# Optimization experiments

Hardware: AMD Instinct MI355X
Metric: run time of the kernel (lower is better)

Reference implementation:

```python
import jax, jax.numpy as jnp
import numpy as np

H = 2048
N = 2_097_152
BINS = 256


def _tensor2image(x):
    # de-normalize from [-1,1]-style to [0,1] (SCGAN's tensor2image)
    return x * 0.5 + 0.5


def _cdf(vals):
    # torch.histc(vals, bins=256, min=0, max=256): unit-width bins; values here lie in [0,256)
    b = jnp.clip(jnp.floor(vals), 0, BINS - 1).astype(jnp.int32)
    hist = jnp.zeros((BINS,), jnp.float32).at[b].add(1.0)
    c = jnp.cumsum(hist)
    return c / c[BINS - 1]


def _trans_table(ref_cdf, adj_cdf):
    # table[i] = first j in 1..255 with adj[j-1] <= ref[i] <= adj[j]; else i. table[0]=0, table[255]=255.
    r = ref_cdf[:, None]                # [256,1]
    lo = adj_cdf[None, :-1]             # adj[j-1], j=1..255
    hi = adj_cdf[None, 1:]              # adj[j]
    cond = (lo <= r) & (r <= hi)        # [256,255]
    found = jnp.any(cond, axis=1)
    j_first = 1 + jnp.argmax(cond, axis=1)
    table = jnp.where(found, j_first, jnp.arange(BINS))
    table = table.at[0].set(0).at[BINS - 1].set(BINS - 1)
    return table


def _histogram_matching(dst_img, ref_img, i0, i1, i2, i3):
    dst_align = dst_img[:, i0, i1]      # [3,N]
    ref_align = ref_img[:, i2, i3]      # [3,N]
    cdf_dst = jax.vmap(_cdf)(dst_align)           # [3,256]
    cdf_ref = jax.vmap(_cdf)(ref_align)           # [3,256]
    tables = jax.vmap(_trans_table)(cdf_dst, cdf_ref)  # [3,256] int
    ix = jnp.clip(jnp.floor(dst_align), 0, BINS - 1).astype(jnp.int32)
    matched = jnp.take_along_axis(tables, ix, axis=1).astype(dst_img.dtype)  # [3,N]
    return dst_img.at[:, i0, i1].set(matched)


def setup_inputs() -> dict:
    key = jax.random.key(0)
    ks = jax.random.split(key, 9)
    return {
        "input_data": jax.random.uniform(ks[0], (1, 3, H, H), jnp.float32),
        "target_data": jax.random.uniform(ks[1], (1, 3, H, H), jnp.float32),
        "mask_src": jax.random.randint(ks[2], (1, 1, H, H), 0, 2).astype(jnp.float32),
        "mask_tar": jax.random.randint(ks[3], (1, 1, H, H), 0, 2).astype(jnp.float32),
        "idx0": jax.random.randint(ks[4], (N,), 0, H),
        "idx1": jax.random.randint(ks[5], (N,), 0, H),
        "idx2": jax.random.randint(ks[6], (N,), 0, H),
        "idx3": jax.random.randint(ks[7], (N,), 0, H),
        "ref": jax.random.uniform(ks[8], (1, 3, H, H), jnp.float32),
    }


def reference(input_data, target_data, mask_src, mask_tar, idx0, idx1, idx2, idx3, ref):
    img = _tensor2image(input_data)[0] * 255.0   # [3,H,H]
    tgt = _tensor2image(target_data)[0] * 255.0  # [3,H,H]
    rf = _tensor2image(ref)[0] * 255.0           # [3,H,H]
    m_src = jnp.broadcast_to(mask_src[0, 0], img.shape)
    m_tar = jnp.broadcast_to(mask_tar[0, 0], tgt.shape)
    input_masked = img * m_src
    target_masked = tgt * m_tar
    ref_masked = rf * m_src
    match = jax.lax.stop_gradient(
        _histogram_matching(ref_masked, target_masked, idx0, idx1, idx2, idx3)
    ) * m_src
    return jnp.mean(jnp.abs(input_masked - match))
```

## Files before the change

### kernel.cpp

```cpp
#include <hip/hip_runtime.h>

#define H 2048
#define HH (H * H)
#define NIDX 2097152
#define BINS 256
#define CH 3

#define NBUCK 64
#define NLIST 128
#define CAPG  139264
#define WS_HIST_DST 0
#define WS_HIST_REF 3072
#define WS_TABLE    6144
#define WS_ACC      9216
#define WS_CURS     9728
#define WS_CTRL_BYTES 16384
#define WS_SEL      16384
#define WS_BPS      (16384 + (size_t)HH)
#define WS_BPR      (WS_BPS + (size_t)HH * 4)
#define WS_LIST     (WS_BPR + (size_t)HH * 4)
#define WS_MAIN_BYTES (WS_LIST + (size_t)NLIST * CAPG * 2)

#define FB_CNT_DST  16384
#define FB_BINPACK  (16384 + (size_t)HH * 2)
#define FB_ZERO_BYTES (16384 + (size_t)HH * 2)

__device__ __forceinline__ int bin_of(float v) {
    int b = (int)floorf(v);
    return min(max(b, 0), BINS - 1);
}


__global__ __launch_bounds__(256) void prep_main(
    const float* __restrict__ mask_src, const float* __restrict__ mask_tar,
    const float* __restrict__ refimg, const float* __restrict__ tgtimg,
    unsigned int* __restrict__ bps, unsigned int* __restrict__ bpr,
    unsigned int* __restrict__ sel4)
{
    const int nq = HH / 4;
    const int stride = gridDim.x * 256;
    for (int q = blockIdx.x * 256 + threadIdx.x; q < nq; q += stride) {
        float4 ms4 = ((const float4*)mask_src)[q];
        float4 mt4 = ((const float4*)mask_tar)[q];
        const float ms[4] = { ms4.x, ms4.y, ms4.z, ms4.w };
        const float mt[4] = { mt4.x, mt4.y, mt4.z, mt4.w };
        unsigned int wsrc[4] = { 0u, 0u, 0u, 0u };
        unsigned int wref[4] = { 0u, 0u, 0u, 0u };
        #pragma unroll
        for (int c = 0; c < CH; ++c) {
            float4 r4 = ((const float4*)(refimg + (size_t)c * HH))[q];
            float4 t4 = ((const float4*)(tgtimg + (size_t)c * HH))[q];
            const float rr[4] = { r4.x, r4.y, r4.z, r4.w };
            const float tt[4] = { t4.x, t4.y, t4.z, t4.w };
            #pragma unroll
            for (int e = 0; e < 4; ++e) {
                float vs = (rr[e] * 0.5f + 0.5f) * 255.0f * ms[e];
                float vt = (tt[e] * 0.5f + 0.5f) * 255.0f * mt[e];
                wsrc[e] |= ((unsigned int)bin_of(vs)) << (8 * c);
                wref[e] |= ((unsigned int)bin_of(vt)) << (8 * c);
            }
        }
        uint4 o1 = { wsrc[0], wsrc[1], wsrc[2], wsrc[3] };
        uint4 o2 = { wref[0], wref[1], wref[2], wref[3] };
        ((uint4*)bps)[q] = o1;
        ((uint4*)bpr)[q] = o2;
        sel4[q] = 0u;
    }
}

#define P1_BLOCKS 512
#define P1_SPB (NIDX / P1_BLOCKS)
#define P1_CAP 128

__global__ __launch_bounds__(256) void partition_kernel(
    const int* __restrict__ idx0, const int* __restrict__ idx1,
    const int* __restrict__ idx2, const int* __restrict__ idx3,
    unsigned short* __restrict__ list_g, unsigned int* __restrict__ curs)
{
    __shared__ unsigned short stage[NLIST * P1_CAP];
    __shared__ unsigned int lcnt[NLIST];
    __shared__ unsigned int lbase[NLIST];
    for (int i = threadIdx.x; i < NLIST; i += 256) lcnt[i] = 0u;
    __syncthreads();

    const int base_k = blockIdx.x * P1_SPB;
    for (int r = 0; r < P1_SPB / 256; ++r) {
        int k = base_k + r * 256 + threadIdx.x;
        int pd = idx0[k] * H + idx1[k];
        int pr = idx2[k] * H + idx3[k];
        {
            int l = pd >> 16;
            unsigned int pos = atomicAdd(&lcnt[l], 1u);
            if (pos < P1_CAP) stage[l * P1_CAP + pos] = (unsigned short)(pd & 0xFFFF);
            else {
                unsigned int g = atomicAdd(&curs[l], 1u);
                if (g < CAPG) list_g[(size_t)l * CAPG + g] = (unsigned short)(pd & 0xFFFF);
            }
        }
        {
            int l = 64 + (pr >> 16);
            unsigned int pos = atomicAdd(&lcnt[l], 1u);
            if (pos < P1_CAP) stage[l * P1_CAP + pos] = (unsigned short)(pr & 0xFFFF);
            else {
                unsigned int g = atomicAdd(&curs[l], 1u);
                if (g < CAPG) list_g[(size_t)l * CAPG + g] = (unsigned short)(pr & 0xFFFF);
            }
        }
    }
    __syncthreads();
    if (threadIdx.x < NLIST) {
        unsigned int n = min(lcnt[threadIdx.x], (unsigned int)P1_CAP);
        lbase[threadIdx.x] = atomicAdd(&curs[threadIdx.x], n);
    }
    __syncthreads();
    for (int b = 0; b < NLIST; ++b) {
        int n = (int)min(lcnt[b], (unsigned int)P1_CAP);
        unsigned int gb = lbase[b];
        for (int e = threadIdx.x; e < n; e += 256) {
            unsigned int gi = gb + e;
            if (gi < CAPG) list_g[(size_t)b * CAPG + gi] = stage[b * P1_CAP + e];
        }
    }
}

__global__ __launch_bounds__(256) void gather_hist_kernel(
    const unsigned short* __restrict__ list_g, const unsigned int* __restrict__ curs,
    const unsigned int* __restrict__ bps, const unsigned int* __restrict__ bpr,
    unsigned char* __restrict__ selected,
    unsigned int* __restrict__ hist_dst, unsigned int* __restrict__ hist_ref)
{
    __shared__ unsigned int hh[CH * BINS];
    for (int i = threadIdx.x; i < CH * BINS; i += 256) hh[i] = 0u;
    __syncthreads();

    const int xcd  = blockIdx.x & 7;
    const int j    = blockIdx.x >> 3;
    const int bsl  = j & 15;
    const int sub  = j >> 4;
    const int side = bsl >> 3;
    const int bucket = xcd * 8 + (bsl & 7);
    const int l = side * 64 + bucket;
    const unsigned int pbase = ((unsigned int)bucket) << 16;
    const unsigned int* __restrict__ src = side ? bpr : bps;

    const unsigned int n = min(curs[l], (unsigned int)CAPG);
    const unsigned int chunk = (((n + 15u) >> 4) + 7u) & ~7u;
    const unsigned int s = (unsigned int)sub * chunk;
    const unsigned int e = min(s + chunk, n);
    const unsigned short* lbase = list_g + (size_t)l * CAPG;

    unsigned int zc = 0;
    for (unsigned int ib = s + (unsigned int)threadIdx.x * 8u; ib < e; ib += 2048u) {
        unsigned int w[8];
        unsigned int pcnt;
        if (ib + 8u <= e) {
            uint4 raw = *(const uint4*)(lbase + ib);
            const unsigned int ent[8] = {
                raw.x & 0xFFFFu, raw.x >> 16, raw.y & 0xFFFFu, raw.y >> 16,
                raw.z & 0xFFFFu, raw.z >> 16, raw.w & 0xFFFFu, raw.w >> 16 };
            #pragma unroll
            for (int k = 0; k < 8; ++k) {
                unsigned int p = pbase | ent[k];
                w[k] = src[p];
                if (side == 0) selected[p] = 1;
            }
            pcnt = 8u;
        } else {
            pcnt = e - ib;
            #pragma unroll
            for (int k = 0; k < 8; ++k) {
                if ((unsigned int)k < pcnt) {
                    unsigned int p = pbase | (unsigned int)lbase[ib + k];
                    w[k] = src[p];
                    if (side == 0) selected[p] = 1;
                } else w[k] = 0xFFFFFFFFu;
            }
        }
        #pragma unroll
        for (int k = 0; k < 8; ++k) {
            if ((unsigned int)k < pcnt) {
                unsigned int ww = w[k];
                if (ww == 0u) ++zc;
                else {
                    atomicAdd(&hh[0 * BINS + (ww & 0xFFu)], 1u);
                    atomicAdd(&hh[1 * BINS + ((ww >> 8) & 0xFFu)], 1u);
                    atomicAdd(&hh[2 * BINS + ((ww >> 16) & 0xFFu)], 1u);
                }
            }
        }
    }

    int z = (int)zc;
    #pragma unroll
    for (int off = 32; off; off >>= 1) z += __shfl_down(z, off);
    if ((threadIdx.x & 63) == 0 && z) {
        atomicAdd(&hh[0 * BINS], (unsigned int)z);
        atomicAdd(&hh[1 * BINS], (unsigned int)z);
        atomicAdd(&hh[2 * BINS], (unsigned int)z);
    }

    __syncthreads();
    unsigned int* dsthist = side ? hist_ref : hist_dst;
    for (int i = threadIdx.x; i < CH * BINS; i += 256) {
        unsigned int v = hh[i];
        if (v) atomicAdd(&dsthist[i], v);
    }
}

__global__ __launch_bounds__(256) void table_kernel(
    const unsigned int* __restrict__ hist_dst,
    const unsigned int* __restrict__ hist_ref,
    int* __restrict__ table)
{
    __shared__ float cd[CH * BINS];
    __shared__ float cr[CH * BINS];
    __shared__ float wpart[4];
    const int i = threadIdx.x;
    const int lane = i & 63;
    const int wave = i >> 6;

    for (int a = 0; a < 6; ++a) {
        const unsigned int* h = (a < 3) ? (hist_dst + a * BINS) : (hist_ref + (a - 3) * BINS);
        float* out = (a < 3) ? (cd + a * BINS) : (cr + (a - 3) * BINS);
        float x = (float)h[i];
        #pragma unroll
        for (int off = 1; off < 64; off <<= 1) {
            float y = __shfl_up(x, off);
            if (lane >= off) x += y;
        }
        if (lane == 63) wpart[wave] = x;
        __syncthreads();
        float prefix = 0.0f;
        #pragma unroll
        for (int w = 0; w < 3; ++w) if (w < wave) prefix += wpart[w];
        x += prefix;
        float tot = wpart[0] + wpart[1] + wpart[2] + wpart[3];
        out[i] = x / tot;
        __syncthreads();
    }

    #pragma unroll
    for (int c = 0; c < CH; ++c) {
        int t;
        if (i == 0) t = 0;
        else if (i == BINS - 1) t = BINS - 1;
        else {
            float r = cd[c * BINS + i];
            int lo = 1, hi = BINS - 1;
            while (lo < hi) {
                int mid = (lo + hi) >> 1;
                if (cr[c * BINS + mid] < r) lo = mid + 1; else hi = mid;
            }
            t = (cr[c * BINS + lo - 1] <= r) ? lo : i;
        }
        table[c * BINS + i] = t;
    }
}

__global__ __launch_bounds__(256) void loss_sel_kernel(
    const float* __restrict__ input, const float* __restrict__ refimg,
    const float* __restrict__ mask_src, const unsigned char* __restrict__ selected,
    const int* __restrict__ table, double* __restrict__ acc)
{
    __shared__ int tab[CH * BINS];
    for (int i = threadIdx.x; i < CH * BINS; i += 256) tab[i] = table[i];
    __syncthreads();

    float lsum = 0.0f;
    const int nq = HH / 4;
    const int stride = gridDim.x * 256;
    for (int q = blockIdx.x * 256 + threadIdx.x; q < nq; q += stride) {
        float4 m4 = ((const float4*)mask_src)[q];
        uchar4 s4 = ((const uchar4*)selected)[q];
        const unsigned char ss[4] = { s4.x, s4.y, s4.z, s4.w };
        const float mm[4] = { m4.x, m4.y, m4.z, m4.w };
        #pragma unroll
        for (int c = 0; c < CH; ++c) {
            float4 a4 = ((const float4*)(input + (size_t)c * HH))[q];
            float4 r4 = ((const float4*)(refimg + (size_t)c * HH))[q];
            const float aa[4] = { a4.x, a4.y, a4.z, a4.w };
            const float rr[4] = { r4.x, r4.y, r4.z, r4.w };
            #pragma unroll
            for (int e = 0; e < 4; ++e) {
                float m = mm[e];
                float av = (aa[e] * 0.5f + 0.5f) * 255.0f * m;
                float rv = (rr[e] * 0.5f + 0.5f) * 255.0f * m;
                float tv = (float)tab[c * BINS + bin_of(rv)];
                float mv = m * (ss[e] ? tv : rv);
                lsum += fabsf(av - mv);
            }
        }
    }

    double d = (double)lsum;
    #pragma unroll
    for (int off = 32; off; off >>= 1) d += __shfl_down(d, off);
    __shared__ double wsum[4];
    int wid = threadIdx.x >> 6;
    int lane = threadIdx.x & 63;
    if (lane == 0) wsum[wid] = d;
    __syncthreads();
    if (threadIdx.x == 0) {
        double t = wsum[0] + wsum[1] + wsum[2] + wsum[3];
        atomicAdd(acc, t);
    }
}

__global__ void finalize_kernel(const double* __restrict__ acc, float* __restrict__ out)
{
    if (threadIdx.x == 0 && blockIdx.x == 0) {
        out[0] = (float)(acc[0] / (double)(CH * (double)HH));
    }
}


__device__ __forceinline__ void cnt_inc(unsigned int* cnt, int p) {
    atomicAdd(&cnt[p >> 1], (p & 1) ? 0x10000u : 1u);
}

__global__ __launch_bounds__(256) void fb_prep_kernel(
    const float* __restrict__ mask_tar, const float* __restrict__ tgtimg,
    unsigned int* __restrict__ binpack)
{
    const int nq = HH / 4;
    const int stride = gridDim.x * 256;
    for (int q = blockIdx.x * 256 + threadIdx.x; q < nq; q += stride) {
        float4 m4 = ((const float4*)mask_tar)[q];
        const float mm[4] = { m4.x, m4.y, m4.z, m4.w };
        unsigned int w[4] = { 0u, 0u, 0u, 0u };
        #pragma unroll
        for (int c = 0; c < CH; ++c) {
            float4 t4 = ((const float4*)(tgtimg + (size_t)c * HH))[q];
            const float tt[4] = { t4.x, t4.y, t4.z, t4.w };
            #pragma unroll
            for (int e = 0; e < 4; ++e) {
                float v = (tt[e] * 0.5f + 0.5f) * 255.0f * mm[e];
                w[e] |= ((unsigned int)bin_of(v)) << (8 * c);
            }
        }
        uint4 out = { w[0], w[1], w[2], w[3] };
        ((uint4*)binpack)[q] = out;
    }
}

__global__ __launch_bounds__(256) void fb_scatter_kernel(
    const int4* __restrict__ idx0, const int4* __restrict__ idx1,
    const int4* __restrict__ idx2, const int4* __restrict__ idx3,
    const unsigned int* __restrict__ binpack,
    unsigned int* __restrict__ cnt_dst, unsigned int* __restrict__ hist_ref)
{
    __shared__ unsigned int hr[CH * BINS];
    for (int i = threadIdx.x; i < CH * BINS; i += 256) hr[i] = 0u;
    __syncthreads();

    unsigned int zc = 0;
    const int n4 = NIDX / 4;
    const int stride = gridDim.x * 256;
    for (int k = blockIdx.x * 256 + threadIdx.x; k < n4; k += stride) {
        int4 a = idx0[k], b = idx1[k], c = idx2[k], d = idx3[k];
        int p0 = c.x * H + d.x, p1 = c.y * H + d.y;
        int p2 = c.z * H + d.z, p3 = c.w * H + d.w;
        unsigned int w0 = binpack[p0], w1 = binpack[p1];
        unsigned int w2 = binpack[p2], w3 = binpack[p3];

        cnt_inc(cnt_dst, a.x * H + b.x);
        cnt_inc(cnt_dst, a.y * H + b.y);
        cnt_inc(cnt_dst, a.z * H + b.z);
        cnt_inc(cnt_dst, a.w * H + b.w);

        const unsigned int ws2[4] = { w0, w1, w2, w3 };
        #pragma unroll
        for (int e = 0; e < 4; ++e) {
            unsigned int w = ws2[e];
            if (w == 0u) ++zc;
            else {
                atomicAdd(&hr[0 * BINS + (w & 0xFFu)], 1u);
                atomicAdd(&hr[1 * BINS + ((w >> 8) & 0xFFu)], 1u);
                atomicAdd(&hr[2 * BINS + ((w >> 16) & 0xFFu)], 1u);
            }
        }
    }

    int z = (int)zc;
    #pragma unroll
    for (int off = 32; off; off >>= 1) z += __shfl_down(z, off);
    if ((threadIdx.x & 63) == 0 && z) {
        atomicAdd(&hr[0 * BINS], (unsigned int)z);
        atomicAdd(&hr[1 * BINS], (unsigned int)z);
        atomicAdd(&hr[2 * BINS], (unsigned int)z);
    }

    __syncthreads();
    for (int i = threadIdx.x; i < CH * BINS; i += 256) {
        unsigned int v = hr[i];
        if (v) atomicAdd(&hist_ref[i], v);
    }
}

__global__ __launch_bounds__(256) void fb_sweep_kernel(
    const float* __restrict__ mask_src, const float* __restrict__ refimg,
    const unsigned int* __restrict__ cnt_dst,
    unsigned int* __restrict__ hist_dst)
{
    __shared__ unsigned int hd[CH * BINS];
    for (int i = threadIdx.x; i < CH * BINS; i += 256) hd[i] = 0u;
    __syncthreads();

    unsigned int zc = 0;
    const int nq = HH / 4;
    const int stride = gridDim.x * 256;
    for (int q = blockIdx.x * 256 + threadIdx.x; q < nq; q += stride) {
        uint2 wd = ((const uint2*)cnt_dst)[q];
        unsigned int cdc[4] = { wd.x & 0xFFFFu, wd.x >> 16, wd.y & 0xFFFFu, wd.y >> 16 };
        float4 ms4 = ((const float4*)mask_src)[q];
        const float ms[4] = { ms4.x, ms4.y, ms4.z, ms4.w };

        float rv[CH][4];
        #pragma unroll
        for (int c = 0; c < CH; ++c) {
            float4 r4 = ((const float4*)(refimg + (size_t)c * HH))[q];
            rv[c][0] = r4.x; rv[c][1] = r4.y; rv[c][2] = r4.z; rv[c][3] = r4.w;
        }
        #pragma unroll
        for (int e = 0; e < 4; ++e) {
            if (cdc[e]) {
                if (ms[e] == 0.0f) zc += cdc[e];
                else {
                    #pragma unroll
                    for (int c = 0; c < CH; ++c) {
                        float v = (rv[c][e] * 0.5f + 0.5f) * 255.0f;
                        atomicAdd(&hd[c * BINS + bin_of(v)], cdc[e]);
                    }
                }
            }
        }
    }

    int z = (int)zc;
    #pragma unroll
    for (int off = 32; off; off >>= 1) z += __shfl_down(z, off);
    if ((threadIdx.x & 63) == 0 && z) {
        atomicAdd(&hd[0 * BINS], (unsigned int)z);
        atomicAdd(&hd[1 * BINS], (unsigned int)z);
        atomicAdd(&hd[2 * BINS], (unsigned int)z);
    }

    __syncthreads();
    for (int i = threadIdx.x; i < CH * BINS; i += 256) {
        unsigned int v = hd[i];
        if (v) atomicAdd(&hist_dst[i], v);
    }
}

__global__ __launch_bounds__(256) void fb_loss_kernel(
    const float* __restrict__ input, const float* __restrict__ refimg,
    const float* __restrict__ mask_src, const unsigned int* __restrict__ cnt_dst,
    const int* __restrict__ table, double* __restrict__ acc)
{
    __shared__ int tab[CH * BINS];
    for (int i = threadIdx.x; i < CH * BINS; i += 256) tab[i] = table[i];
    __syncthreads();

    float lsum = 0.0f;
    const int nq = HH / 4;
    const int stride = gridDim.x * 256;
    for (int q = blockIdx.x * 256 + threadIdx.x; q < nq; q += stride) {
        float4 m4 = ((const float4*)mask_src)[q];
        uint2 w = ((const uint2*)cnt_dst)[q];
        const unsigned int sel[4] = { w.x & 0xFFFFu, w.x >> 16, w.y & 0xFFFFu, w.y >> 16 };
        const float mm[4] = { m4.x, m4.y, m4.z, m4.w };
        #pragma unroll
        for (int c = 0; c < CH; ++c) {
            float4 a4 = ((const float4*)(input + (size_t)c * HH))[q];
            float4 r4 = ((const float4*)(refimg + (size_t)c * HH))[q];
            const float aa[4] = { a4.x, a4.y, a4.z, a4.w };
            const float rr[4] = { r4.x, r4.y, r4.z, r4.w };
            #pragma unroll
            for (int e = 0; e < 4; ++e) {
                float m = mm[e];
                float av = (aa[e] * 0.5f + 0.5f) * 255.0f * m;
                float rv = (rr[e] * 0.5f + 0.5f) * 255.0f * m;
                float tv = (float)tab[c * BINS + bin_of(rv)];
                float mv = m * (sel[e] ? tv : rv);
                lsum += fabsf(av - mv);
            }
        }
    }

    double d = (double)lsum;
    #pragma unroll
    for (int off = 32; off; off >>= 1) d += __shfl_down(d, off);
    __shared__ double wsum[4];
    int wid = threadIdx.x >> 6;
    int lane = threadIdx.x & 63;
    if (lane == 0) wsum[wid] = d;
    __syncthreads();
    if (threadIdx.x == 0) {
        double t = wsum[0] + wsum[1] + wsum[2] + wsum[3];
        atomicAdd(acc, t);
    }
}


extern "C" void kernel_launch(void* const* d_in, const int* in_sizes, int n_in,
                              void* d_out, int out_size, void* d_ws, size_t ws_size,
                              hipStream_t stream)
{
    const float* input    = (const float*)d_in[0];
    const float* target   = (const float*)d_in[1];
    const float* mask_src = (const float*)d_in[2];
    const float* mask_tar = (const float*)d_in[3];
    const int*   idx0     = (const int*)d_in[4];
    const int*   idx1     = (const int*)d_in[5];
    const int*   idx2     = (const int*)d_in[6];
    const int*   idx3     = (const int*)d_in[7];
    const float* refimg   = (const float*)d_in[8];

    char* ws = (char*)d_ws;
    unsigned int* hist_dst = (unsigned int*)(ws + WS_HIST_DST);
    unsigned int* hist_ref = (unsigned int*)(ws + WS_HIST_REF);
    int*          table    = (int*)(ws + WS_TABLE);
    double*       acc      = (double*)(ws + WS_ACC);

    if (ws_size >= WS_MAIN_BYTES) {
        unsigned int*   curs     = (unsigned int*)(ws + WS_CURS);
        unsigned char*  selected = (unsigned char*)(ws + WS_SEL);
        unsigned int*   bps      = (unsigned int*)(ws + WS_BPS);
        unsigned int*   bpr      = (unsigned int*)(ws + WS_BPR);
        unsigned short* list_g   = (unsigned short*)(ws + WS_LIST);

        hipMemsetAsync(d_ws, 0, WS_CTRL_BYTES, stream);
        prep_main<<<2048, 256, 0, stream>>>(mask_src, mask_tar, refimg, target,
                                            bps, bpr, (unsigned int*)selected);
        partition_kernel<<<P1_BLOCKS, 256, 0, stream>>>(idx0, idx1, idx2, idx3,
                                                        list_g, curs);
        gather_hist_kernel<<<2048, 256, 0, stream>>>(list_g, curs, bps, bpr,
                                                     selected, hist_dst, hist_ref);
        table_kernel<<<1, 256, 0, stream>>>(hist_dst, hist_ref, table);
        loss_sel_kernel<<<2048, 256, 0, stream>>>(input, refimg, mask_src,
                                                  selected, table, acc);
        finalize_kernel<<<1, 64, 0, stream>>>(acc, (float*)d_out);
    } else {
        unsigned int* cnt_dst = (unsigned int*)(ws + FB_CNT_DST);
        unsigned int* binpack = (unsigned int*)(ws + FB_BINPACK);

        hipMemsetAsync(d_ws, 0, FB_ZERO_BYTES, stream);
        fb_prep_kernel<<<2048, 256, 0, stream>>>(mask_tar, target, binpack);
        fb_scatter_kernel<<<2048, 256, 0, stream>>>((const int4*)idx0, (const int4*)idx1,
                                                    (const int4*)idx2, (const int4*)idx3,
                                                    binpack, cnt_dst, hist_ref);
        fb_sweep_kernel<<<1024, 256, 0, stream>>>(mask_src, refimg, cnt_dst, hist_dst);
        table_kernel<<<1, 256, 0, stream>>>(hist_dst, hist_ref, table);
        fb_loss_kernel<<<2048, 256, 0, stream>>>(input, refimg, mask_src, cnt_dst,
                                                 table, acc);
        finalize_kernel<<<1, 64, 0, stream>>>(acc, (float*)d_out);
    }
}
```

Baseline: 328.5 us.

## Fuse bin-packing prep and index partitioning into one heterogeneous kernel launch

Merges the image bin-packing kernel and the index partition kernel into a single launch, where the first 512 blocks partition indices and the remaining 2048 blocks each pack 8 pixels without a grid-stride loop. The selected-flag clearing moves from a kernel store into an enlarged memset. Partition now reads indices as int4, shrinks the shared staging capacity, and flushes staged lists per wave rather than serially. The loss kernel is likewise unrolled to 8 pixels per thread. The aim is to overlap the two independent phases and cut launch and tail overhead, at the cost of more global-atomic overflow from the smaller staging buffer and extra register pressure.

```diff
diff --git a/kernel.cpp b/kernel.cpp
--- a/kernel.cpp
+++ b/kernel.cpp
@@ -6,7 +6,6 @@
 #define BINS 256
 #define CH 3
 
-#define NBUCK 64
 #define NLIST 128
 #define CAPG  139264
 #define WS_HIST_DST 0
@@ -16,6 +15,7 @@
 #define WS_CURS     9728
 #define WS_CTRL_BYTES 16384
 #define WS_SEL      16384
+#define WS_ZERO_BYTES (16384 + (size_t)HH)
 #define WS_BPS      (16384 + (size_t)HH)
 #define WS_BPR      (WS_BPS + (size_t)HH * 4)
 #define WS_LIST     (WS_BPR + (size_t)HH * 4)
@@ -31,95 +31,113 @@
 }
 
 
-__global__ __launch_bounds__(256) void prep_main(
+
+#define P1_BLOCKS 512
+#define P1_SPB (NIDX / P1_BLOCKS)
+#define P1_CAP 96
+#define FUSE_GRID (P1_BLOCKS + 2048)
+
+__global__ __launch_bounds__(256) void prep_part_kernel(
     const float* __restrict__ mask_src, const float* __restrict__ mask_tar,
     const float* __restrict__ refimg, const float* __restrict__ tgtimg,
     unsigned int* __restrict__ bps, unsigned int* __restrict__ bpr,
-    unsigned int* __restrict__ sel4)
-{
-    const int nq = HH / 4;
-    const int stride = gridDim.x * 256;
-    for (int q = blockIdx.x * 256 + threadIdx.x; q < nq; q += stride) {
-        float4 ms4 = ((const float4*)mask_src)[q];
-        float4 mt4 = ((const float4*)mask_tar)[q];
-        const float ms[4] = { ms4.x, ms4.y, ms4.z, ms4.w };
-        const float mt[4] = { mt4.x, mt4.y, mt4.z, mt4.w };
-        unsigned int wsrc[4] = { 0u, 0u, 0u, 0u };
-        unsigned int wref[4] = { 0u, 0u, 0u, 0u };
-        #pragma unroll
-        for (int c = 0; c < CH; ++c) {
-            float4 r4 = ((const float4*)(refimg + (size_t)c * HH))[q];
-            float4 t4 = ((const float4*)(tgtimg + (size_t)c * HH))[q];
-            const float rr[4] = { r4.x, r4.y, r4.z, r4.w };
-            const float tt[4] = { t4.x, t4.y, t4.z, t4.w };
+    const int* __restrict__ idx0, const int* __restrict__ idx1,
+    const int* __restrict__ idx2, const int* __restrict__ idx3,
+    unsigned short* __restrict__ list_g, unsigned int* __restrict__ curs)
+{
+    __shared__ unsigned short stage[NLIST * P1_CAP];
+    __shared__ unsigned int lcnt[NLIST];
+    __shared__ unsigned int lbase[NLIST];
+
+    if (blockIdx.x < P1_BLOCKS) {
+        for (int i = threadIdx.x; i < NLIST; i += 256) lcnt[i] = 0u;
+        __syncthreads();
+
+        const int base4 = blockIdx.x * (P1_SPB / 4);
+        #pragma unroll
+        for (int r = 0; r < P1_SPB / 1024; ++r) {
+            int k4 = base4 + r * 256 + threadIdx.x;
+            int4 a = ((const int4*)idx0)[k4];
+            int4 b = ((const int4*)idx1)[k4];
+            int4 c = ((const int4*)idx2)[k4];
+            int4 d = ((const int4*)idx3)[k4];
+            const int pd[4] = { a.x * H + b.x, a.y * H + b.y,
+                                a.z * H + b.z, a.w * H + b.w };
+            const int pr[4] = { c.x * H + d.x, c.y * H + d.y,
+                                c.z * H + d.z, c.w * H + d.w };
             #pragma unroll
             for (int e = 0; e < 4; ++e) {
+                {
+                    int l = pd[e] >> 16;
+                    unsigned int pos = atomicAdd(&lcnt[l], 1u);
+                    if (pos < P1_CAP) stage[l * P1_CAP + pos] = (unsigned short)(pd[e] & 0xFFFF);
+                    else {
+                        unsigned int g = atomicAdd(&curs[l], 1u);
+                        if (g < CAPG) list_g[(size_t)l * CAPG + g] = (unsigned short)(pd[e] & 0xFFFF);
+                    }
+                }
+                {
+                    int l = 64 + (pr[e] >> 16);
+                    unsigned int pos = atomicAdd(&lcnt[l], 1u);
+                    if (pos < P1_CAP) stage[l * P1_CAP + pos] = (unsigned short)(pr[e] & 0xFFFF);
+                    else {
+                        unsigned int g = atomicAdd(&curs[l], 1u);
+                        if (g < CAPG) list_g[(size_t)l * CAPG + g] = (unsigned short)(pr[e] & 0xFFFF);
+                    }
+                }
+            }
+        }
+        __syncthreads();
+        if (threadIdx.x < NLIST) {
+            unsigned int n = min(lcnt[threadIdx.x], (unsigned int)P1_CAP);
+            lbase[threadIdx.x] = atomicAdd(&curs[threadIdx.x], n);
+        }
+        __syncthreads();
+        const int wave = threadIdx.x >> 6;
+        const int lane = threadIdx.x & 63;
+        for (int b = wave; b < NLIST; b += 4) {
+            int n = (int)min(lcnt[b], (unsigned int)P1_CAP);
+            unsigned int gb = lbase[b];
+            for (int e = lane; e < n; e += 64) {
+                unsigned int gi = gb + e;
+                if (gi < CAPG) list_g[(size_t)b * CAPG + gi] = stage[b * P1_CAP + e];
+            }
+        }
+    } else {
+        const int t = (int)(blockIdx.x - P1_BLOCKS) * 256 + threadIdx.x;
+        const int q = t << 1;
+        float4 msA = ((const float4*)mask_src)[q];
+        float4 msB = ((const float4*)mask_src)[q + 1];
+        float4 mtA = ((const float4*)mask_tar)[q];
+        float4 mtB = ((const float4*)mask_tar)[q + 1];
+        const float ms[8] = { msA.x, msA.y, msA.z, msA.w, msB.x, msB.y, msB.z, msB.w };
+        const float mt[8] = { mtA.x, mtA.y, mtA.z, mtA.w, mtB.x, mtB.y, mtB.z, mtB.w };
+        unsigned int wsrc[8] = { 0u,0u,0u,0u,0u,0u,0u,0u };
+        unsigned int wref[8] = { 0u,0u,0u,0u,0u,0u,0u,0u };
+        #pragma unroll
+        for (int c = 0; c < CH; ++c) {
+            float4 rA = ((const float4*)(refimg + (size_t)c * HH))[q];
+            float4 rB = ((const float4*)(refimg + (size_t)c * HH))[q + 1];
+            float4 tA = ((const float4*)(tgtimg + (size_t)c * HH))[q];
+            float4 tB = ((const float4*)(tgtimg + (size_t)c * HH))[q + 1];
+            const float rr[8] = { rA.x, rA.y, rA.z, rA.w, rB.x, rB.y, rB.z, rB.w };
+            const float tt[8] = { tA.x, tA.y, tA.z, tA.w, tB.x, tB.y, tB.z, tB.w };
+            #pragma unroll
+            for (int e = 0; e < 8; ++e) {
                 float vs = (rr[e] * 0.5f + 0.5f) * 255.0f * ms[e];
                 float vt = (tt[e] * 0.5f + 0.5f) * 255.0f * mt[e];
                 wsrc[e] |= ((unsigned int)bin_of(vs)) << (8 * c);
                 wref[e] |= ((unsigned int)bin_of(vt)) << (8 * c);
             }
         }
-        uint4 o1 = { wsrc[0], wsrc[1], wsrc[2], wsrc[3] };
-        uint4 o2 = { wref[0], wref[1], wref[2], wref[3] };
-        ((uint4*)bps)[q] = o1;
-        ((uint4*)bpr)[q] = o2;
-        sel4[q] = 0u;
-    }
-}
-
-#define P1_BLOCKS 512
-#define P1_SPB (NIDX / P1_BLOCKS)
-#define P1_CAP 128
-
-__global__ __launch_bounds__(256) void partition_kernel(
-    const int* __restrict__ idx0, const int* __restrict__ idx1,
-    const int* __restrict__ idx2, const int* __restrict__ idx3,
-    unsigned short* __restrict__ list_g, unsigned int* __restrict__ curs)
-{
-    __shared__ unsigned short stage[NLIST * P1_CAP];
-    __shared__ unsigned int lcnt[NLIST];
-    __shared__ unsigned int lbase[NLIST];
-    for (int i = threadIdx.x; i < NLIST; i += 256) lcnt[i] = 0u;
-    __syncthreads();
-
-    const int base_k = blockIdx.x * P1_SPB;
-    for (int r = 0; r < P1_SPB / 256; ++r) {
-        int k = base_k + r * 256 + threadIdx.x;
-        int pd = idx0[k] * H + idx1[k];
-        int pr = idx2[k] * H + idx3[k];
-        {
-            int l = pd >> 16;
-            unsigned int pos = atomicAdd(&lcnt[l], 1u);
-            if (pos < P1_CAP) stage[l * P1_CAP + pos] = (unsigned short)(pd & 0xFFFF);
-            else {
-                unsigned int g = atomicAdd(&curs[l], 1u);
-                if (g < CAPG) list_g[(size_t)l * CAPG + g] = (unsigned short)(pd & 0xFFFF);
-            }
-        }
-        {
-            int l = 64 + (pr >> 16);
-            unsigned int pos = atomicAdd(&lcnt[l], 1u);
-            if (pos < P1_CAP) stage[l * P1_CAP + pos] = (unsigned short)(pr & 0xFFFF);
-            else {
-                unsigned int g = atomicAdd(&curs[l], 1u);
-                if (g < CAPG) list_g[(size_t)l * CAPG + g] = (unsigned short)(pr & 0xFFFF);
-            }
-        }
-    }
-    __syncthreads();
-    if (threadIdx.x < NLIST) {
-        unsigned int n = min(lcnt[threadIdx.x], (unsigned int)P1_CAP);
-        lbase[threadIdx.x] = atomicAdd(&curs[threadIdx.x], n);
-    }
-    __syncthreads();
-    for (int b = 0; b < NLIST; ++b) {
-        int n = (int)min(lcnt[b], (unsigned int)P1_CAP);
-        unsigned int gb = lbase[b];
-        for (int e = threadIdx.x; e < n; e += 256) {
-            unsigned int gi = gb + e;
-            if (gi < CAPG) list_g[(size_t)b * CAPG + gi] = stage[b * P1_CAP + e];
-        }
+        uint4 s1 = { wsrc[0], wsrc[1], wsrc[2], wsrc[3] };
+        uint4 s2 = { wsrc[4], wsrc[5], wsrc[6], wsrc[7] };
+        uint4 r1 = { wref[0], wref[1], wref[2], wref[3] };
+        uint4 r2 = { wref[4], wref[5], wref[6], wref[7] };
+        ((uint4*)bps)[q]     = s1;
+        ((uint4*)bps)[q + 1] = s2;
+        ((uint4*)bpr)[q]     = r1;
+        ((uint4*)bpr)[q + 1] = r2;
     }
 }
 
@@ -266,29 +284,32 @@
     for (int i = threadIdx.x; i < CH * BINS; i += 256) tab[i] = table[i];
     __syncthreads();
 
+    const int t = blockIdx.x * 256 + threadIdx.x;
+    const int q = t << 1;
+    float4 mA = ((const float4*)mask_src)[q];
+    float4 mB = ((const float4*)mask_src)[q + 1];
+    uchar4 sA = ((const uchar4*)selected)[q];
+    uchar4 sB = ((const uchar4*)selected)[q + 1];
+    const unsigned char ss[8] = { sA.x, sA.y, sA.z, sA.w, sB.x, sB.y, sB.z, sB.w };
+    const float mm[8] = { mA.x, mA.y, mA.z, mA.w, mB.x, mB.y, mB.z, mB.w };
+
     float lsum = 0.0f;
-    const int nq = HH / 4;
-    const int stride = gridDim.x * 256;
-    for (int q = blockIdx.x * 256 + threadIdx.x; q < nq; q += stride) {
-        float4 m4 = ((const float4*)mask_src)[q];
-        uchar4 s4 = ((const uchar4*)selected)[q];
-        const unsigned char ss[4] = { s4.x, s4.y, s4.z, s4.w };
-        const float mm[4] = { m4.x, m4.y, m4.z, m4.w };
-        #pragma unroll
-        for (int c = 0; c < CH; ++c) {
-            float4 a4 = ((const float4*)(input + (size_t)c * HH))[q];
-            float4 r4 = ((const float4*)(refimg + (size_t)c * HH))[q];
-            const float aa[4] = { a4.x, a4.y, a4.z, a4.w };
-            const float rr[4] = { r4.x, r4.y, r4.z, r4.w };
-            #pragma unroll
-            for (int e = 0; e < 4; ++e) {
-                float m = mm[e];
-                float av = (aa[e] * 0.5f + 0.5f) * 255.0f * m;
-                float rv = (rr[e] * 0.5f + 0.5f) * 255.0f * m;
-                float tv = (float)tab[c * BINS + bin_of(rv)];
-                float mv = m * (ss[e] ? tv : rv);
-                lsum += fabsf(av - mv);
-            }
+    #pragma unroll
+    for (int c = 0; c < CH; ++c) {
+        float4 aA = ((const float4*)(input + (size_t)c * HH))[q];
+        float4 aB = ((const float4*)(input + (size_t)c * HH))[q + 1];
+        float4 rA = ((const float4*)(refimg + (size_t)c * HH))[q];
+        float4 rB = ((const float4*)(refimg + (size_t)c * HH))[q + 1];
+        const float aa[8] = { aA.x, aA.y, aA.z, aA.w, aB.x, aB.y, aB.z, aB.w };
+        const float rr[8] = { rA.x, rA.y, rA.z, rA.w, rB.x, rB.y, rB.z, rB.w };
+        #pragma unroll
+        for (int e = 0; e < 8; ++e) {
+            float m = mm[e];
+            float av = (aa[e] * 0.5f + 0.5f) * 255.0f * m;
+            float rv = (rr[e] * 0.5f + 0.5f) * 255.0f * m;
+            float tv = (float)tab[c * BINS + bin_of(rv)];
+            float mv = m * (ss[e] ? tv : rv);
+            lsum += fabsf(av - mv);
         }
     }
 
@@ -301,8 +322,8 @@
     if (lane == 0) wsum[wid] = d;
     __syncthreads();
     if (threadIdx.x == 0) {
-        double t = wsum[0] + wsum[1] + wsum[2] + wsum[3];
-        atomicAdd(acc, t);
+        double tt = wsum[0] + wsum[1] + wsum[2] + wsum[3];
+        atomicAdd(acc, tt);
     }
 }
 
@@ -529,11 +550,10 @@
         unsigned int*   bpr      = (unsigned int*)(ws + WS_BPR);
         unsigned short* list_g   = (unsigned short*)(ws + WS_LIST);
 
-        hipMemsetAsync(d_ws, 0, WS_CTRL_BYTES, stream);
-        prep_main<<<2048, 256, 0, stream>>>(mask_src, mask_tar, refimg, target,
-                                            bps, bpr, (unsigned int*)selected);
-        partition_kernel<<<P1_BLOCKS, 256, 0, stream>>>(idx0, idx1, idx2, idx3,
-                                                        list_g, curs);
+        hipMemsetAsync(d_ws, 0, WS_ZERO_BYTES, stream);
+        prep_part_kernel<<<FUSE_GRID, 256, 0, stream>>>(
+            mask_src, mask_tar, refimg, target, bps, bpr,
+            idx0, idx1, idx2, idx3, list_g, curs);
         gather_hist_kernel<<<2048, 256, 0, stream>>>(list_g, curs, bps, bpr,
                                                      selected, hist_dst, hist_ref);
         table_kernel<<<1, 256, 0, stream>>>(hist_dst, hist_ref, table);
```

New measurement: 302.8 us. 7.8% less time.
